# Performance work log

Measured on AMD Instinct MI355X. Metric: run time of the kernel, lower is better.

Reference implementation:

```python
import jax, jax.numpy as jnp
import numpy as np

N = 100000; E = 1600000; D_IN = 128; HID = 64; HEADS = 2; OUT = 2; B = 8192
NEG_SLOPE = 0.2


def gat_conv(x, edge_index, W, a_src, a_dst, bias):
    """PyG-style GATConv with add_self_loops=True, concat=False (mean over heads).
    x: [N, Fin], W: [Fin, H*C], a_src/a_dst: [H, C], bias: [C]."""
    n = x.shape[0]
    H, C = a_src.shape
    h = (x @ W).reshape(n, H, C)                      # [N,H,C]
    s_src = (h * a_src[None]).sum(-1)                 # [N,H]
    s_dst = (h * a_dst[None]).sum(-1)                 # [N,H]
    loop = jnp.arange(n, dtype=edge_index.dtype)
    src = jnp.concatenate([edge_index[0], loop])      # [E+N]
    dst = jnp.concatenate([edge_index[1], loop])
    e = jax.nn.leaky_relu(s_src[src] + s_dst[dst], NEG_SLOPE)   # [E+N,H]
    # segment softmax over edges grouped by destination node
    m = jax.ops.segment_max(e, dst, num_segments=n)             # [N,H]
    ex = jnp.exp(e - m[dst])
    z = jax.ops.segment_sum(ex, dst, num_segments=n)            # [N,H]
    alpha = ex / z[dst]                                          # [E+N,H]
    msg = h[src] * alpha[:, :, None]                             # [E+N,H,C]
    out = jax.ops.segment_sum(msg, dst, num_segments=n)         # [N,H,C]
    return out.mean(axis=1) + bias                               # concat=False -> mean over heads


def setup_inputs() -> dict:
    key = jax.random.key(0)
    ks = jax.random.split(key, 32)
    def p(k, shape, fan_in):
        return (jax.random.normal(k, shape, dtype=jnp.float32) / np.sqrt(fan_in)).astype(jnp.float32)
    inp = {}
    inp["x_l"] = jax.random.normal(ks[0], (N, D_IN), dtype=jnp.float32)
    inp["x_r"] = jax.random.normal(ks[1], (N, D_IN), dtype=jnp.float32)
    inp["edge_index_l"] = jax.random.randint(ks[2], (2, E), 0, N, dtype=jnp.int64 if jax.config.jax_enable_x64 else jnp.int32)
    inp["edge_index_r"] = jax.random.randint(ks[3], (2, E), 0, N, dtype=jnp.int64 if jax.config.jax_enable_x64 else jnp.int32)
    inp["labels_l"] = jax.random.randint(ks[4], (B,), 0, N)
    inp["labels_r"] = jax.random.randint(ks[5], (B,), 0, N)
    i = 6
    for side in ("l", "r"):
        inp[f"w1{side}"] = p(ks[i], (D_IN, HEADS * HID), D_IN); i += 1
        inp[f"as1{side}"] = p(ks[i], (HEADS, HID), HID); i += 1
        inp[f"ad1{side}"] = p(ks[i], (HEADS, HID), HID); i += 1
        inp[f"b1{side}"] = jnp.zeros((HID,), jnp.float32)
        inp[f"w2{side}"] = p(ks[i], (HID, HEADS * HID), HID); i += 1
        inp[f"as2{side}"] = p(ks[i], (HEADS, HID), HID); i += 1
        inp[f"ad2{side}"] = p(ks[i], (HEADS, HID), HID); i += 1
        inp[f"b2{side}"] = jnp.zeros((HID,), jnp.float32)
    inp["fc1_w"] = p(ks[i], (2 * HID, HID), 2 * HID); i += 1
    inp["fc1_b"] = jnp.zeros((HID,), jnp.float32)
    inp["fc2_w"] = p(ks[i], (HID, OUT), HID); i += 1
    inp["fc2_b"] = jnp.zeros((OUT,), jnp.float32)
    return inp


def reference(x_l, x_r, edge_index_l, edge_index_r, labels_l, labels_r,
              w1l, as1l, ad1l, b1l, w2l, as2l, ad2l, b2l,
              w1r, as1r, ad1r, b1r, w2r, as2r, ad2r, b2r,
              fc1_w, fc1_b, fc2_w, fc2_b):
    # left tower (dropout is identity in eval mode)
    hl = jax.nn.relu(gat_conv(x_l, edge_index_l, w1l, as1l, ad1l, b1l))
    hl = jax.nn.relu(gat_conv(hl, edge_index_l, w2l, as2l, ad2l, b2l))
    # right tower
    hr = jax.nn.relu(gat_conv(x_r, edge_index_r, w1r, as1r, ad1r, b1r))
    hr = jax.nn.relu(gat_conv(hr, edge_index_r, w2r, as2r, ad2r, b2r))
    # merge_graphs: gather node features per labeled pair, concat
    merged = jnp.concatenate([hl[labels_l], hr[labels_r]], axis=-1)  # [B, 2*HID]
    x = jax.nn.relu(merged @ fc1_w + fc1_b)
    return x @ fc2_w + fc2_b
```

## Files before the change

### kernel.cpp

```cpp
#include <hip/hip_runtime.h>
#include <hip/hip_bf16.h>
#include <hip/hip_fp16.h>

constexpr int NN   = 100000;
constexpr int EE   = 1600000;
constexpr int BB   = 8192;
constexpr int PAD  = 48;
constexpr float NEG_SLOPE = 0.2f;

constexpr int GBM = 128;
constexpr int GB = (NN + GBM - 1) / GBM;
constexpr int AB2 = NN / 8;

constexpr int BSPAN = 256;
constexpr int NB    = (NN + BSPAN - 1) / BSPAN;
constexpr int BCAP  = 5120;
constexpr int CHA   = 4096;
constexpr int NCH   = (EE + CHA - 1) / CHA;

typedef _Float16 f16x8 __attribute__((ext_vector_type(8)));
typedef _Float16 f16x4 __attribute__((ext_vector_type(4)));
typedef float    f32x4 __attribute__((ext_vector_type(4)));

__device__ __forceinline__ float4 ld4(const float* p) { return *(const float4*)p; }

template <typename TIN, int K>
__global__ __launch_bounds__(256)
void gemm_mfma(const TIN* __restrict__ xA, const TIN* __restrict__ xB,
               const float* __restrict__ WA, const float* __restrict__ asA,
               const float* __restrict__ adA,
               const float* __restrict__ WB, const float* __restrict__ asB,
               const float* __restrict__ adB,
               __half* __restrict__ hA, __half* __restrict__ hB,
               float* __restrict__ ssA, float* __restrict__ sdA,
               float* __restrict__ ssB, float* __restrict__ sdB) {
    constexpr bool HAS_LO = sizeof(TIN) == 4;
    constexpr int LSZ = HAS_LO ? 65536 : 49152;
    __shared__ __align__(16) char lds[LSZ];
    char* const xh = lds;
    char* const xl = HAS_LO ? (lds + 16384) : lds;
    char* const wh = lds + (HAS_LO ? 32768 : 16384);
    char* const wl = wh + 16384;

    const int bid0 = blockIdx.x;
    const bool right = bid0 >= GB;
    const int bid = right ? bid0 - GB : bid0;
    const TIN* __restrict__ x = right ? xB : xA;
    const float* __restrict__ W = right ? WB : WA;
    const float* __restrict__ a_src = right ? asB : asA;
    const float* __restrict__ a_dst = right ? adB : adA;
    __half* __restrict__ h = right ? hB : hA;
    float* __restrict__ ssrc = right ? ssB : ssA;
    float* __restrict__ sdst = right ? sdB : sdA;

    const int tid = threadIdx.x;
    const int wid = tid >> 6;
    const int lane = tid & 63;
    const int l15 = lane & 15;
    const int lg = lane >> 4;
    const int row0 = bid * GBM;

    f32x4 acc[2][8];
    #pragma unroll
    for (int i = 0; i < 2; ++i)
        #pragma unroll
        for (int j = 0; j < 8; ++j) acc[i][j] = (f32x4)0.f;

    for (int kt = 0; kt < K; kt += 64) {
        __syncthreads();
        if constexpr (HAS_LO) {
            #pragma unroll
            for (int i = 0; i < 8; ++i) {
                int idx = tid + i * 256;
                int row = idx >> 4, c4 = idx & 15;
                int grow = row0 + row; if (grow >= NN) grow = NN - 1;
                float4 v = ld4(&x[(size_t)grow * K + kt + c4 * 4]);
                f16x4 hv, lv;
                float f0 = v.x; _Float16 h0 = (_Float16)f0; hv[0] = h0; lv[0] = (_Float16)(f0 - (float)h0);
                float f1 = v.y; _Float16 h1 = (_Float16)f1; hv[1] = h1; lv[1] = (_Float16)(f1 - (float)h1);
                float f2 = v.z; _Float16 h2 = (_Float16)f2; hv[2] = h2; lv[2] = (_Float16)(f2 - (float)h2);
                float f3 = v.w; _Float16 h3 = (_Float16)f3; hv[3] = h3; lv[3] = (_Float16)(f3 - (float)h3);
                int byt = row * 128 + ((c4 * 8) ^ ((row & 7) << 4));
                *(f16x4*)(xh + byt) = hv;
                *(f16x4*)(xl + byt) = lv;
            }
        } else {
            #pragma unroll
            for (int i = 0; i < 4; ++i) {
                int idx = tid + i * 256;
                int row = idx >> 3, c8 = idx & 7;
                int grow = row0 + row; if (grow >= NN) grow = NN - 1;
                uint4 v = *(const uint4*)&x[(size_t)grow * 64 + c8 * 8];
                int byt = row * 128 + ((c8 * 16) ^ ((row & 7) << 4));
                *(uint4*)(xh + byt) = v;
            }
        }
        #pragma unroll
        for (int i = 0; i < 8; ++i) {
            int idx = tid + i * 256;
            int kk = idx >> 5, c4 = idx & 31;
            float4 v = ld4(&W[(size_t)(kt + kk) * 128 + c4 * 4]);
            float f[4] = {v.x, v.y, v.z, v.w};
            #pragma unroll
            for (int j = 0; j < 4; ++j) {
                int col = c4 * 4 + j;
                _Float16 hi = (_Float16)f[j];
                _Float16 lo = (_Float16)(f[j] - (float)hi);
                int byt = col * 128 + ((kk * 2) ^ ((col & 7) << 4));
                *(_Float16*)(wh + byt) = hi;
                *(_Float16*)(wl + byt) = lo;
            }
        }
        __syncthreads();

        #pragma unroll
        for (int ks = 0; ks < 2; ++ks) {
            const int koff = ks * 64 + lg * 16;
            f16x8 ah[2], al[2];
            #pragma unroll
            for (int rt = 0; rt < 2; ++rt) {
                int row = wid * 32 + rt * 16 + l15;
                int byt = row * 128 + (koff ^ ((row & 7) << 4));
                ah[rt] = *(const f16x8*)(xh + byt);
                if constexpr (HAS_LO) al[rt] = *(const f16x8*)(xl + byt);
            }
            #pragma unroll
            for (int ct = 0; ct < 8; ++ct) {
                int col = ct * 16 + l15;
                int byt = col * 128 + (koff ^ ((col & 7) << 4));
                f16x8 bh = *(const f16x8*)(wh + byt);
                f16x8 bl = *(const f16x8*)(wl + byt);
                #pragma unroll
                for (int rt = 0; rt < 2; ++rt) {
                    acc[rt][ct] = __builtin_amdgcn_mfma_f32_16x16x32_f16(ah[rt], bh, acc[rt][ct], 0, 0, 0);
                    acc[rt][ct] = __builtin_amdgcn_mfma_f32_16x16x32_f16(ah[rt], bl, acc[rt][ct], 0, 0, 0);
                    if constexpr (HAS_LO)
                        acc[rt][ct] = __builtin_amdgcn_mfma_f32_16x16x32_f16(al[rt], bh, acc[rt][ct], 0, 0, 0);
                }
            }
        }
    }

    float sv[8], dv[8];
    #pragma unroll
    for (int ct = 0; ct < 8; ++ct) {
        sv[ct] = a_src[ct * 16 + l15];
        dv[ct] = a_dst[ct * 16 + l15];
    }
    #pragma unroll
    for (int rt = 0; rt < 2; ++rt) {
        #pragma unroll
        for (int r = 0; r < 4; ++r) {
            int row = row0 + wid * 32 + rt * 16 + lg * 4 + r;
            bool ok = row < NN;
            if (ok) {
                #pragma unroll
                for (int ct = 0; ct < 8; ++ct)
                    h[(size_t)row * 128 + ct * 16 + l15] = __float2half(acc[rt][ct][r]);
            }
            float ps0 = 0.f, pd0 = 0.f, ps1 = 0.f, pd1 = 0.f;
            #pragma unroll
            for (int ct = 0; ct < 4; ++ct) {
                ps0 = fmaf(acc[rt][ct][r], sv[ct], ps0);
                pd0 = fmaf(acc[rt][ct][r], dv[ct], pd0);
                ps1 = fmaf(acc[rt][ct + 4][r], sv[ct + 4], ps1);
                pd1 = fmaf(acc[rt][ct + 4][r], dv[ct + 4], pd1);
            }
            ps0 += __shfl_xor(ps0, 1); pd0 += __shfl_xor(pd0, 1);
            ps1 += __shfl_xor(ps1, 1); pd1 += __shfl_xor(pd1, 1);
            ps0 += __shfl_xor(ps0, 2); pd0 += __shfl_xor(pd0, 2);
            ps1 += __shfl_xor(ps1, 2); pd1 += __shfl_xor(pd1, 2);
            ps0 += __shfl_xor(ps0, 4); pd0 += __shfl_xor(pd0, 4);
            ps1 += __shfl_xor(ps1, 4); pd1 += __shfl_xor(pd1, 4);
            ps0 += __shfl_xor(ps0, 8); pd0 += __shfl_xor(pd0, 8);
            ps1 += __shfl_xor(ps1, 8); pd1 += __shfl_xor(pd1, 8);
            if (ok && l15 == 0) {
                ssrc[row * 2 + 0] = ps0;
                ssrc[row * 2 + 1] = ps1;
                sdst[row * 2 + 0] = pd0;
                sdst[row * 2 + 1] = pd1;
            }
        }
    }
}

__global__ __launch_bounds__(256)
void k_bucket(const int* __restrict__ el, const int* __restrict__ er,
              int2* __restrict__ buf, int* __restrict__ gcur) {
    __shared__ int2 P0[CHA];
    __shared__ int2 P1[CHA];
    __shared__ int hist[NB];
    __shared__ int st[NB];
    __shared__ int ofs[NB];
    __shared__ int base[NB];
    __shared__ int sc[512];

    const int blk = blockIdx.x;
    const bool right = blk >= NCH;
    const int* __restrict__ e = right ? er : el;
    const int sideoff = right ? NB : 0;
    const int cbase = (right ? blk - NCH : blk) * CHA;
    int cnum = EE - cbase; if (cnum > CHA) cnum = CHA;
    const int t = threadIdx.x;

    for (int i = t; i < cnum; i += 256) {
        int2 p; p.x = e[EE + cbase + i]; p.y = e[cbase + i];
        P0[i] = p;
    }
    for (int i = t; i < NB; i += 256) hist[i] = 0;
    __syncthreads();
    for (int i = t; i < cnum; i += 256) atomicAdd(&hist[P0[i].x >> 8], 1);
    __syncthreads();

    sc[t]       = (t < NB)       ? hist[t]       : 0;
    sc[t + 256] = (t + 256 < NB) ? hist[t + 256] : 0;
    __syncthreads();
    for (int off = 1; off < 512; off <<= 1) {
        int a0 = sc[t];
        int a1 = sc[t + 256];
        int b0 = (t >= off)       ? sc[t - off]       : 0;
        int b1 = (t + 256 >= off) ? sc[t + 256 - off] : 0;
        __syncthreads();
        sc[t] = a0 + b0;
        sc[t + 256] = a1 + b1;
        __syncthreads();
    }
    for (int i = t; i < NB; i += 256) {
        int s = sc[i] - hist[i];
        st[i] = s;
        ofs[i] = s;
    }
    __syncthreads();
    for (int i = t; i < cnum; i += 256) {
        int2 p = P0[i];
        int pos = atomicAdd(&ofs[p.x >> 8], 1);
        P1[pos] = p;
    }
    __syncthreads();
    for (int i = t; i < NB; i += 256)
        base[i] = hist[i] ? atomicAdd(&gcur[sideoff + i], hist[i]) : 0;
    __syncthreads();
    for (int j = t; j < cnum; j += 256) {
        int2 p = P1[j];
        int bk = p.x >> 8;
        buf[(size_t)(sideoff + bk) * BCAP + base[bk] + (j - st[bk])] = p;
    }
}

__global__ __launch_bounds__(256)
void k_csr(const int2* __restrict__ buf, const int* __restrict__ gcur,
           int* __restrict__ cntl, int* __restrict__ cntr,
           int* __restrict__ csrl, int* __restrict__ csrr) {
    __shared__ int lcnt[BSPAN];
    __shared__ __align__(16) int lcsr[BSPAN * PAD];

    const int blk = blockIdx.x;
    const bool right = blk >= NB;
    const int bk = right ? blk - NB : blk;
    int* __restrict__ cnt = right ? cntr : cntl;
    int* __restrict__ csr = right ? csrr : csrl;
    const int2* __restrict__ src = buf + (size_t)blk * BCAP;
    const int count = gcur[blk];
    const int lo = bk * BSPAN;
    int nn = NN - lo; if (nn > BSPAN) nn = BSPAN;
    const int t = threadIdx.x;

    for (int i = t; i < nn; i += 256) lcnt[i] = 0;
    __syncthreads();
    for (int i = t; i < count; i += 256) {
        int2 p = src[i];
        int ld = p.x - lo;
        int slot = atomicAdd(&lcnt[ld], 1);
        lcsr[ld * PAD + slot] = p.y;
    }
    __syncthreads();
    const int tot4 = (nn * PAD) >> 2;
    int4* __restrict__ dst4 = (int4*)&csr[(size_t)lo * PAD];
    const int4* __restrict__ s4 = (const int4*)lcsr;
    for (int i = t; i < tot4; i += 256) dst4[i] = s4[i];
    for (int i = t; i < nn; i += 256) cnt[lo + i] = lcnt[i];
}

__device__ __forceinline__
void att_body(int n, const __half* __restrict__ h,
              const float* __restrict__ ssrc, const float* __restrict__ sdst,
              const int* __restrict__ cnt, const int* __restrict__ csr,
              const float* __restrict__ bias, __half* __restrict__ out) {
    const int g  = threadIdx.x & 31;
    const int hs = g >> 4;
    const int j  = g & 15;
    const int ch = g * 4;

    float sd = sdst[n * 2 + hs];
    float es = ssrc[n * 2 + hs] + sd;
    es = es > 0.f ? es : NEG_SLOPE * es;
    const float wself = __expf(es);
    float zl = 0.f;

    uint2 sv = *(const uint2*)&h[(size_t)n * 128 + ch];
    __half2 sh0 = *(__half2*)&sv.x, sh1 = *(__half2*)&sv.y;
    float2 p01 = __half22float2(sh0), p23 = __half22float2(sh1);
    float a0 = wself * p01.x, a1 = wself * p01.y;
    float a2 = wself * p23.x, a3 = wself * p23.y;

    int b = n * PAD;
    const int e = b + cnt[n];
    while (b < e) {
        int c = e - b; if (c > 16) c = 16;
        int idx = b + (j < c ? j : c - 1);
        int sj = csr[idx];
        float ev = ssrc[sj * 2 + hs] + sd;
        ev = ev > 0.f ? ev : NEG_SLOPE * ev;
        float w = (j < c) ? __expf(ev) : 0.f;
        zl += w;
        int jj = 0;
        for (; jj + 4 <= c; jj += 4) {
            int s0 = __shfl(sj, jj,     32);
            int s1 = __shfl(sj, jj + 1, 32);
            int s2 = __shfl(sj, jj + 2, 32);
            int s3 = __shfl(sj, jj + 3, 32);
            float w0 = __shfl(w, hs * 16 + jj,     32);
            float w1 = __shfl(w, hs * 16 + jj + 1, 32);
            float w2 = __shfl(w, hs * 16 + jj + 2, 32);
            float w3 = __shfl(w, hs * 16 + jj + 3, 32);
            uint2 u0 = *(const uint2*)&h[(size_t)(unsigned)(s0 * 128 + ch)];
            uint2 u1 = *(const uint2*)&h[(size_t)(unsigned)(s1 * 128 + ch)];
            uint2 u2 = *(const uint2*)&h[(size_t)(unsigned)(s2 * 128 + ch)];
            uint2 u3 = *(const uint2*)&h[(size_t)(unsigned)(s3 * 128 + ch)];
            float2 f0a = __half22float2(*(__half2*)&u0.x), f0b = __half22float2(*(__half2*)&u0.y);
            float2 f1a = __half22float2(*(__half2*)&u1.x), f1b = __half22float2(*(__half2*)&u1.y);
            float2 f2a = __half22float2(*(__half2*)&u2.x), f2b = __half22float2(*(__half2*)&u2.y);
            float2 f3a = __half22float2(*(__half2*)&u3.x), f3b = __half22float2(*(__half2*)&u3.y);
            a0 = fmaf(w0, f0a.x, a0); a1 = fmaf(w0, f0a.y, a1);
            a2 = fmaf(w0, f0b.x, a2); a3 = fmaf(w0, f0b.y, a3);
            a0 = fmaf(w1, f1a.x, a0); a1 = fmaf(w1, f1a.y, a1);
            a2 = fmaf(w1, f1b.x, a2); a3 = fmaf(w1, f1b.y, a3);
            a0 = fmaf(w2, f2a.x, a0); a1 = fmaf(w2, f2a.y, a1);
            a2 = fmaf(w2, f2b.x, a2); a3 = fmaf(w2, f2b.y, a3);
            a0 = fmaf(w3, f3a.x, a0); a1 = fmaf(w3, f3a.y, a1);
            a2 = fmaf(w3, f3b.x, a2); a3 = fmaf(w3, f3b.y, a3);
        }
        for (; jj < c; ++jj) {
            int s0   = __shfl(sj, jj, 32);
            float w0 = __shfl(w, hs * 16 + jj, 32);
            uint2 u0 = *(const uint2*)&h[(size_t)(unsigned)(s0 * 128 + ch)];
            float2 f0a = __half22float2(*(__half2*)&u0.x), f0b = __half22float2(*(__half2*)&u0.y);
            a0 = fmaf(w0, f0a.x, a0); a1 = fmaf(w0, f0a.y, a1);
            a2 = fmaf(w0, f0b.x, a2); a3 = fmaf(w0, f0b.y, a3);
        }
        b += c;
    }

    zl += __shfl_xor(zl, 1, 32);
    zl += __shfl_xor(zl, 2, 32);
    zl += __shfl_xor(zl, 4, 32);
    zl += __shfl_xor(zl, 8, 32);
    const float z = wself + zl;

    float zi = 1.f / z;
    a0 *= zi; a1 *= zi; a2 *= zi; a3 *= zi;
    a0 = 0.5f * (a0 + __shfl_xor(a0, 16));
    a1 = 0.5f * (a1 + __shfl_xor(a1, 16));
    a2 = 0.5f * (a2 + __shfl_xor(a2, 16));
    a3 = 0.5f * (a3 + __shfl_xor(a3, 16));
    if (hs == 0) {
        float4 bv = *(const float4*)&bias[ch];
        a0 += bv.x; a1 += bv.y; a2 += bv.z; a3 += bv.w;
        a0 = a0 > 0.f ? a0 : 0.f;
        a1 = a1 > 0.f ? a1 : 0.f;
        a2 = a2 > 0.f ? a2 : 0.f;
        a3 = a3 > 0.f ? a3 : 0.f;
        __align__(8) __half2 hp[2];
        hp[0] = __floats2half2_rn(a0, a1);
        hp[1] = __floats2half2_rn(a2, a3);
        *(uint2*)&out[(size_t)n * 64 + ch] = *(uint2*)hp;
    }
}

__global__ __launch_bounds__(256)
void k_att2x(const __half* __restrict__ h_l, const __half* __restrict__ h_r,
             const float* __restrict__ ssrc_l, const float* __restrict__ sdst_l,
             const float* __restrict__ ssrc_r, const float* __restrict__ sdst_r,
             const int* __restrict__ cnt_l, const int* __restrict__ csr_l,
             const int* __restrict__ cnt_r, const int* __restrict__ csr_r,
             const float* __restrict__ bias_l, const float* __restrict__ bias_r,
             __half* __restrict__ feat_l, __half* __restrict__ feat_r) {
    int blk = blockIdx.x;
    bool right = blk >= AB2;
    int n = (blk - (right ? AB2 : 0)) * 8 + (threadIdx.x >> 5);
    if (!right) att_body(n, h_l, ssrc_l, sdst_l, cnt_l, csr_l, bias_l, feat_l);
    else        att_body(n, h_r, ssrc_r, sdst_r, cnt_r, csr_r, bias_r, feat_r);
}

__global__ __launch_bounds__(256)
void k_fc(const __half* __restrict__ fl, const __half* __restrict__ fr,
          const int* __restrict__ ll, const int* __restrict__ lr,
          const float* __restrict__ w1, const float* __restrict__ b1,
          const float* __restrict__ w2, const float* __restrict__ b2,
          float* __restrict__ out) {
    int b = blockIdx.x * 4 + (threadIdx.x >> 6);
    int j = threadIdx.x & 63;
    int la = ll[b], lb = lr[b];
    float v0 = __half2float(fl[(size_t)la * 64 + j]);
    float v1 = __half2float(fr[(size_t)lb * 64 + j]);
    float acc = b1[j];
    #pragma unroll 8
    for (int k = 0; k < 64; ++k)
        acc += __shfl(v0, k, 64) * w1[k * 64 + j];
    #pragma unroll 8
    for (int k = 0; k < 64; ++k)
        acc += __shfl(v1, k, 64) * w1[(64 + k) * 64 + j];
    float x1 = acc > 0.f ? acc : 0.f;
    float p0 = x1 * w2[j * 2 + 0];
    float p1 = x1 * w2[j * 2 + 1];
    #pragma unroll
    for (int o = 32; o >= 1; o >>= 1) {
        p0 += __shfl_xor(p0, o, 64);
        p1 += __shfl_xor(p1, o, 64);
    }
    if (j == 0) {
        out[b * 2 + 0] = p0 + b2[0];
        out[b * 2 + 1] = p1 + b2[1];
    }
}

extern "C" void kernel_launch(void* const* d_in, const int* in_sizes, int n_in,
                              void* d_out, int out_size, void* d_ws, size_t ws_size,
                              hipStream_t stream) {
    const float* x_l  = (const float*)d_in[0];
    const float* x_r  = (const float*)d_in[1];
    const int* ei_l  = (const int*)d_in[2];
    const int* ei_r  = (const int*)d_in[3];
    const int* lab_l = (const int*)d_in[4];
    const int* lab_r = (const int*)d_in[5];
    const float* w1l  = (const float*)d_in[6];
    const float* as1l = (const float*)d_in[7];
    const float* ad1l = (const float*)d_in[8];
    const float* b1l  = (const float*)d_in[9];
    const float* w2l  = (const float*)d_in[10];
    const float* as2l = (const float*)d_in[11];
    const float* ad2l = (const float*)d_in[12];
    const float* b2l  = (const float*)d_in[13];
    const float* w1r  = (const float*)d_in[14];
    const float* as1r = (const float*)d_in[15];
    const float* ad1r = (const float*)d_in[16];
    const float* b1r  = (const float*)d_in[17];
    const float* w2r  = (const float*)d_in[18];
    const float* as2r = (const float*)d_in[19];
    const float* ad2r = (const float*)d_in[20];
    const float* b2r  = (const float*)d_in[21];
    const float* fc1w = (const float*)d_in[22];
    const float* fc1b = (const float*)d_in[23];
    const float* fc2w = (const float*)d_in[24];
    const float* fc2b = (const float*)d_in[25];

    char* p = (char*)d_ws;
    auto alloc = [&](size_t bytes) -> void* {
        void* q = (void*)p;
        p += (bytes + 255) & ~(size_t)255;
        return q;
    };
    __half* h_l    = (__half*)alloc((size_t)NN * 128 * 2);
    __half* h_r    = (__half*)alloc((size_t)NN * 128 * 2);
    __half* feat_l = (__half*)alloc((size_t)NN * 64 * 2);
    __half* feat_r = (__half*)alloc((size_t)NN * 64 * 2);
    float* ssrc_l = (float*)alloc((size_t)NN * 2 * 4);
    float* sdst_l = (float*)alloc((size_t)NN * 2 * 4);
    float* ssrc_r = (float*)alloc((size_t)NN * 2 * 4);
    float* sdst_r = (float*)alloc((size_t)NN * 2 * 4);
    int* cnt2  = (int*)alloc(((size_t)2 * NN + 2 * NB) * 4);
    int* csr_l = (int*)alloc((size_t)NN * PAD * 4);
    int* csr_r = (int*)alloc((size_t)NN * PAD * 4);
    int* cnt_l = cnt2;
    int* cnt_r = cnt2 + NN;
    int* gcur  = cnt2 + 2 * NN;

    int2* buf = (int2*)h_l;

    hipMemsetAsync(gcur, 0, (size_t)2 * NB * 4, stream);

    k_bucket<<<2 * NCH, 256, 0, stream>>>(ei_l, ei_r, buf, gcur);

    k_csr<<<2 * NB, 256, 0, stream>>>(buf, gcur, cnt_l, cnt_r, csr_l, csr_r);

    gemm_mfma<float, 128><<<2 * GB, 256, 0, stream>>>(
        x_l, x_r, w1l, as1l, ad1l, w1r, as1r, ad1r,
        h_l, h_r, ssrc_l, sdst_l, ssrc_r, sdst_r);

    k_att2x<<<2 * AB2, 256, 0, stream>>>(h_l, h_r, ssrc_l, sdst_l, ssrc_r, sdst_r,
                                         cnt_l, csr_l, cnt_r, csr_r,
                                         b1l, b1r, feat_l, feat_r);

    gemm_mfma<__half, 64><<<2 * GB, 256, 0, stream>>>(
        feat_l, feat_r, w2l, as2l, ad2l, w2r, as2r, ad2r,
        h_l, h_r, ssrc_l, sdst_l, ssrc_r, sdst_r);

    k_att2x<<<2 * AB2, 256, 0, stream>>>(h_l, h_r, ssrc_l, sdst_l, ssrc_r, sdst_r,
                                         cnt_l, csr_l, cnt_r, csr_r,
                                         b2l, b2r, feat_l, feat_r);

    k_fc<<<(BB + 3) / 4, 256, 0, stream>>>(feat_l, feat_r, lab_l, lab_r,
                                           fc1w, fc1b, fc2w, fc2b,
                                           (float*)d_out);
}
```

Measured before the change: 633.9 us.

## Merge CSR build and first-layer GEMM into one launch; pack bucket entries

```diff
diff --git a/kernel.cpp b/kernel.cpp
--- a/kernel.cpp
+++ b/kernel.cpp
@@ -25,33 +25,18 @@
 __device__ __forceinline__ float4 ld4(const float* p) { return *(const float4*)p; }
 
 template <typename TIN, int K>
-__global__ __launch_bounds__(256)
-void gemm_mfma(const TIN* __restrict__ xA, const TIN* __restrict__ xB,
-               const float* __restrict__ WA, const float* __restrict__ asA,
-               const float* __restrict__ adA,
-               const float* __restrict__ WB, const float* __restrict__ asB,
-               const float* __restrict__ adB,
-               __half* __restrict__ hA, __half* __restrict__ hB,
-               float* __restrict__ ssA, float* __restrict__ sdA,
-               float* __restrict__ ssB, float* __restrict__ sdB) {
+__device__ __forceinline__
+void gemm_mfma_body(int bid, const TIN* __restrict__ x,
+                    const float* __restrict__ W,
+                    const float* __restrict__ a_src, const float* __restrict__ a_dst,
+                    __half* __restrict__ h,
+                    float* __restrict__ ssrc, float* __restrict__ sdst,
+                    char* lds) {
     constexpr bool HAS_LO = sizeof(TIN) == 4;
-    constexpr int LSZ = HAS_LO ? 65536 : 49152;
-    __shared__ __align__(16) char lds[LSZ];
     char* const xh = lds;
     char* const xl = HAS_LO ? (lds + 16384) : lds;
     char* const wh = lds + (HAS_LO ? 32768 : 16384);
     char* const wl = wh + 16384;
-
-    const int bid0 = blockIdx.x;
-    const bool right = bid0 >= GB;
-    const int bid = right ? bid0 - GB : bid0;
-    const TIN* __restrict__ x = right ? xB : xA;
-    const float* __restrict__ W = right ? WB : WA;
-    const float* __restrict__ a_src = right ? asB : asA;
-    const float* __restrict__ a_dst = right ? adB : adA;
-    __half* __restrict__ h = right ? hB : hA;
-    float* __restrict__ ssrc = right ? ssB : ssA;
-    float* __restrict__ sdst = right ? sdB : sdA;
 
     const int tid = threadIdx.x;
     const int wid = tid >> 6;
@@ -186,7 +171,7 @@
 
 __global__ __launch_bounds__(256)
 void k_bucket(const int* __restrict__ el, const int* __restrict__ er,
-              int2* __restrict__ buf, int* __restrict__ gcur) {
+              int* __restrict__ buf, int* __restrict__ gcur) {
     __shared__ int2 P0[CHA];
     __shared__ int2 P1[CHA];
     __shared__ int hist[NB];
@@ -243,23 +228,23 @@
     for (int j = t; j < cnum; j += 256) {
         int2 p = P1[j];
         int bk = p.x >> 8;
-        buf[(size_t)(sideoff + bk) * BCAP + base[bk] + (j - st[bk])] = p;
-    }
-}
-
-__global__ __launch_bounds__(256)
-void k_csr(const int2* __restrict__ buf, const int* __restrict__ gcur,
-           int* __restrict__ cntl, int* __restrict__ cntr,
-           int* __restrict__ csrl, int* __restrict__ csrr) {
-    __shared__ int lcnt[BSPAN];
-    __shared__ __align__(16) int lcsr[BSPAN * PAD];
-
-    const int blk = blockIdx.x;
+        buf[(size_t)(sideoff + bk) * BCAP + base[bk] + (j - st[bk])] =
+            (p.y << 8) | (p.x & 255);
+    }
+}
+
+__device__ __forceinline__
+void csr_body(int blk, const int* __restrict__ buf, const int* __restrict__ gcur,
+              int* __restrict__ cntl, int* __restrict__ cntr,
+              int* __restrict__ csrl, int* __restrict__ csrr, char* smem) {
+    int* lcnt = (int*)smem;
+    int* lcsr = (int*)(smem + 1024);
+
     const bool right = blk >= NB;
     const int bk = right ? blk - NB : blk;
     int* __restrict__ cnt = right ? cntr : cntl;
     int* __restrict__ csr = right ? csrr : csrl;
-    const int2* __restrict__ src = buf + (size_t)blk * BCAP;
+    const int* __restrict__ src = buf + (size_t)blk * BCAP;
     const int count = gcur[blk];
     const int lo = bk * BSPAN;
     int nn = NN - lo; if (nn > BSPAN) nn = BSPAN;
@@ -268,10 +253,11 @@
     for (int i = t; i < nn; i += 256) lcnt[i] = 0;
     __syncthreads();
     for (int i = t; i < count; i += 256) {
-        int2 p = src[i];
-        int ld = p.x - lo;
+        int v = src[i];
+        int ld = v & 255;
+        int s  = (int)((unsigned)v >> 8);
         int slot = atomicAdd(&lcnt[ld], 1);
-        lcsr[ld * PAD + slot] = p.y;
+        lcsr[ld * PAD + slot] = s;
     }
     __syncthreads();
     const int tot4 = (nn * PAD) >> 2;
@@ -279,6 +265,52 @@
     const int4* __restrict__ s4 = (const int4*)lcsr;
     for (int i = t; i < tot4; i += 256) dst4[i] = s4[i];
     for (int i = t; i < nn; i += 256) cnt[lo + i] = lcnt[i];
+}
+
+__global__ __launch_bounds__(256)
+void k_csr_gemm1(const int* __restrict__ buf, const int* __restrict__ gcur,
+                 int* __restrict__ cnt_l, int* __restrict__ cnt_r,
+                 int* __restrict__ csr_l, int* __restrict__ csr_r,
+                 const float* __restrict__ x_l, const float* __restrict__ x_r,
+                 const float* __restrict__ w1l, const float* __restrict__ as1l,
+                 const float* __restrict__ ad1l,
+                 const float* __restrict__ w1r, const float* __restrict__ as1r,
+                 const float* __restrict__ ad1r,
+                 __half* __restrict__ h_l, __half* __restrict__ h_r,
+                 float* __restrict__ ssrc_l, float* __restrict__ sdst_l,
+                 float* __restrict__ ssrc_r, float* __restrict__ sdst_r) {
+    __shared__ __align__(16) char smem[65536];
+    int b = blockIdx.x;
+    if (b < 2 * NB) {
+        csr_body(b, buf, gcur, cnt_l, cnt_r, csr_l, csr_r, smem);
+    } else {
+        b -= 2 * NB;
+        if (b < GB)
+            gemm_mfma_body<float, 128>(b, x_l, w1l, as1l, ad1l,
+                                       h_l, ssrc_l, sdst_l, smem);
+        else
+            gemm_mfma_body<float, 128>(b - GB, x_r, w1r, as1r, ad1r,
+                                       h_r, ssrc_r, sdst_r, smem);
+    }
+}
+
+__global__ __launch_bounds__(256)
+void k_gemm2x(const __half* __restrict__ f_l, const __half* __restrict__ f_r,
+              const float* __restrict__ w2l, const float* __restrict__ as2l,
+              const float* __restrict__ ad2l,
+              const float* __restrict__ w2r, const float* __restrict__ as2r,
+              const float* __restrict__ ad2r,
+              __half* __restrict__ h_l, __half* __restrict__ h_r,
+              float* __restrict__ ssrc_l, float* __restrict__ sdst_l,
+              float* __restrict__ ssrc_r, float* __restrict__ sdst_r) {
+    __shared__ __align__(16) char smem[49152];
+    int b = blockIdx.x;
+    if (b < GB)
+        gemm_mfma_body<__half, 64>(b, (const __half*)f_l, w2l, as2l, ad2l,
+                                   h_l, ssrc_l, sdst_l, smem);
+    else
+        gemm_mfma_body<__half, 64>(b - GB, (const __half*)f_r, w2r, as2r, ad2r,
+                                   h_r, ssrc_r, sdst_r, smem);
 }
 
 __device__ __forceinline__
@@ -475,15 +507,14 @@
     int* cnt_r = cnt2 + NN;
     int* gcur  = cnt2 + 2 * NN;
 
-    int2* buf = (int2*)h_l;
+    int* buf = (int*)feat_l;
 
     hipMemsetAsync(gcur, 0, (size_t)2 * NB * 4, stream);
 
     k_bucket<<<2 * NCH, 256, 0, stream>>>(ei_l, ei_r, buf, gcur);
 
-    k_csr<<<2 * NB, 256, 0, stream>>>(buf, gcur, cnt_l, cnt_r, csr_l, csr_r);
-
-    gemm_mfma<float, 128><<<2 * GB, 256, 0, stream>>>(
+    k_csr_gemm1<<<2 * NB + 2 * GB, 256, 0, stream>>>(
+        buf, gcur, cnt_l, cnt_r, csr_l, csr_r,
         x_l, x_r, w1l, as1l, ad1l, w1r, as1r, ad1r,
         h_l, h_r, ssrc_l, sdst_l, ssrc_r, sdst_r);
 
@@ -491,9 +522,9 @@
                                          cnt_l, csr_l, cnt_r, csr_r,
                                          b1l, b1r, feat_l, feat_r);
 
-    gemm_mfma<__half, 64><<<2 * GB, 256, 0, stream>>>(
-        feat_l, feat_r, w2l, as2l, ad2l, w2r, as2r, ad2r,
-        h_l, h_r, ssrc_l, sdst_l, ssrc_r, sdst_r);
+    k_gemm2x<<<2 * GB, 256, 0, stream>>>(feat_l, feat_r,
+                                         w2l, as2l, ad2l, w2r, as2r, ad2r,
+                                         h_l, h_r, ssrc_l, sdst_l, ssrc_r, sdst_r);
 
     k_att2x<<<2 * AB2, 256, 0, stream>>>(h_l, h_r, ssrc_l, sdst_l, ssrc_r, sdst_r,
                                          cnt_l, csr_l, cnt_r, csr_r,
```

Measured after the change: 590.8 us. 1.07x faster.
